# Kernel optimization log

Measured on AMD Instinct MI355X. Metric: run time of the kernel, lower is better.

The kernel has to match this reference:

```python
import jax, jax.numpy as jnp
import numpy as np

B, T, D, L = 16, 2048, 512, 2


def setup_inputs() -> dict:
    key = jax.random.key(0)
    k1, k2, k3 = jax.random.split(key, 3)
    scale = 1.0 / np.sqrt(D)
    x = jax.random.normal(k1, (B, T, D), dtype=jnp.float32)
    Wx = jax.random.normal(k2, (L, D, 4 * D), dtype=jnp.float32) * scale
    Wh = jax.random.normal(k3, (L, D, 4 * D), dtype=jnp.float32) * scale
    b = jnp.zeros((L, 4 * D), dtype=jnp.float32)
    return {"x": x, "Wx": Wx, "Wh": Wh, "b": b}


def _lstm_layer(y, Wx_l, Wh_l, b_l):
    # y: [B, T, D]; Wx_l: [D, 4D]; Wh_l: [D, 4D]; b_l: [4D]
    Bn, Tn, Dn = y.shape
    # Precompute input contribution for all timesteps (one big GEMM).
    xg = jnp.einsum('btd,de->bte', y, Wx_l) + b_l  # [B, T, 4D]

    def step(carry, xt):
        h, c = carry
        gates = xt + h @ Wh_l  # [B, 4D]
        i, f, g, o = jnp.split(gates, 4, axis=-1)
        i = jax.nn.sigmoid(i)
        f = jax.nn.sigmoid(f)
        g = jnp.tanh(g)
        o = jax.nn.sigmoid(o)
        c = f * c + i * g
        h = o * jnp.tanh(c)
        return (h, c), h

    h0 = jnp.zeros((Bn, Dn), y.dtype)
    c0 = jnp.zeros((Bn, Dn), y.dtype)
    _, ys = jax.lax.scan(step, (h0, c0), jnp.swapaxes(xg, 0, 1))  # [T, B, D]
    return jnp.swapaxes(ys, 0, 1)


def reference(x, Wx, Wh, b):
    # Stacked LSTM with residual skip (flax LSTMCell gate order i, f, g, o;
    # input kernels have no bias, hidden kernels carry the bias -> single b).
    y = x
    for l in range(Wx.shape[0]):
        y = _lstm_layer(y, Wx[l], Wh[l], b[l])
    return y + x  # skip=1
```

## Files before the change

### kernel.cpp

```cpp
#include <hip/hip_runtime.h>
#include <stdint.h>

#define B_  16
#define T_  2048
#define D_  512

typedef short v8s __attribute__((ext_vector_type(8)));
typedef float v4f __attribute__((ext_vector_type(4)));

#define WT_OFF   0u
#define H0_OFF   8388608u
#define H1_OFF   41943040u
#define XB_OFF   75497472u
#define WS_NEED  (XB_OFF + 33554432u)

#define SENT 0xFFFFFFFFu

__device__ __forceinline__ short f2bf(float f) {
  unsigned u = __builtin_bit_cast(unsigned, f);
  u = (u + 0x7FFFu + ((u >> 16) & 1u)) >> 16;
  return (short)u;
}
__device__ __forceinline__ float sigmoid_fast(float z) { return 1.f / (1.f + __expf(-z)); }
__device__ __forceinline__ float tanh_fast(float z) {
  float e = __expf(2.f * z);
  return 1.f - 2.f / (e + 1.f);
}
__device__ __forceinline__ unsigned long long cohLoadU2(const unsigned* p) {
  return __hip_atomic_load((unsigned long long*)p, __ATOMIC_RELAXED, __HIP_MEMORY_SCOPE_AGENT);
}
__device__ __forceinline__ void cohStoreU(unsigned* p, unsigned v) {
  __hip_atomic_store(p, v, __ATOMIC_RELAXED, __HIP_MEMORY_SCOPE_AGENT);
}

__global__ void prep_weights(const float* __restrict__ Wx, const float* __restrict__ Wh,
                             short* __restrict__ wT) {
  int tid = blockIdx.x * 256 + threadIdx.x;
  int l   = tid >> 21;
  int mat = (tid >> 20) & 1;
  int rem = tid & ((1 << 20) - 1);
  int k   = rem >> 11;
  int col = rem & 2047;
  const float* src = mat ? Wh : Wx;
  float v = src[(l << 20) + (k << 11) + col];
  int q = col >> 9, r9 = col & 511, g = r9 >> 3, jj = r9 & 7;
  int c = q * 8 + jj, ntile = c >> 4, n = c & 15;
  int kap = k >> 5, k5 = k & 31, quad = k5 >> 3, j = k5 & 7;
  int lane = quad * 16 + n;
  int dst = ((((l * 2 + mat) * 64 + g) * 2 + ntile) * 16 + kap) * 512 + lane * 8 + j;
  wT[dst] = f2bf(v);
}

__global__ void prep_x(const float* __restrict__ x, short* __restrict__ xP,
                       unsigned* __restrict__ hwords) {
  int tid = blockIdx.x * 256 + threadIdx.x;
  hwords[tid] = SENT;
  int b = tid >> 20, r = tid & ((1 << 20) - 1), t = r >> 9, d = r & 511;
  xP[(size_t)t * 8192 + (d >> 3) * 128 + b * 8 + (d & 7)] = f2bf(x[tid]);
}

__device__ __forceinline__ unsigned coh_load8(const short* p, v8s afr[8]) {
  unsigned mx = 0;
#pragma unroll
  for (int kk = 0; kk < 8; ++kk) {
    const unsigned* q = (const unsigned*)(p + kk * 512);
    unsigned long long w0 = cohLoadU2(q);
    unsigned long long w1 = cohLoadU2(q + 2);
    unsigned a = (unsigned)w0, b = (unsigned)(w0 >> 32);
    unsigned c = (unsigned)w1, d = (unsigned)(w1 >> 32);
    mx = a > mx ? a : mx;
    mx = b > mx ? b : mx;
    mx = c > mx ? c : mx;
    mx = d > mx ? d : mx;
    uint4 pk; pk.x = a; pk.y = b; pk.z = c; pk.w = d;
    afr[kk] = __builtin_bit_cast(v8s, pk);
  }
  return mx;
}

__device__ __forceinline__ void mfma32(const v8s afr[8], const v8s wfr[4][8], v4f acc[4]) {
#pragma unroll
  for (int kk = 0; kk < 8; ++kk) {
#pragma unroll
    for (int nt = 0; nt < 4; ++nt)
      acc[nt] = __builtin_amdgcn_mfma_f32_16x16x32_bf16(afr[kk], wfr[nt][kk], acc[nt], 0, 0, 0);
  }
}

__global__ __launch_bounds__(256, 1) void lstm_persist(
    const float* __restrict__ x, const short* __restrict__ xP,
    const short* __restrict__ wT, const float* __restrict__ bias,
    short* h0, short* h1, float* __restrict__ out) {
  const int wg   = blockIdx.x;
  const int l    = wg >> 5;
  const int g    = wg & 31;
  const int tid  = threadIdx.x;
  const int wave = tid >> 6;
  const int lane = tid & 63;
  const int m    = wave >> 1;
  const int kh   = wave & 1;
  const int n15  = lane & 15;
  const int quad = lane >> 4;

  __shared__ float LDSG[2][4][16][68];

  short* hOwn = l ? h1 : h0;

  v8s wfr[4][8];
#pragma unroll
  for (int nt = 0; nt < 4; ++nt) {
    const int gOld = 2 * g + (nt >> 1);
    const int nt2  = nt & 1;
    const short* wb = wT + (size_t)((((l * 2 + m) * 64 + gOld) * 2 + nt2) * 16 + kh * 8) * 512 + lane * 8;
#pragma unroll
    for (int kk = 0; kk < 8; ++kk) wfr[nt][kk] = *(const v8s*)(wb + kk * 512);
  }

  const int eIdx = wave * 64 + lane;
  const int bb = eIdx >> 3, jp = eIdx & 7;
  const int hi = jp >> 2;
  const int jj = 2 * (jp & 3);
  float bq[4][2];
#pragma unroll
  for (int q = 0; q < 4; ++q) {
    bq[q][0] = bias[l * 2048 + q * 512 + g * 16 + 2 * jp];
    bq[q][1] = bias[l * 2048 + q * 512 + g * 16 + 2 * jp + 1];
  }
  float c0 = 0.f, c1 = 0.f;

  const int aOff = kh * 4096 + quad * 128 + n15 * 8;

  for (int t = 0; t < T_; ++t) {
    const int buf = t & 1;

    float2 xv;
    size_t xi = 0;
    if (l == 1 && wave < 2) {
      xi = (size_t)bb * (T_ * D_) + (size_t)t * D_ + g * 16 + 2 * jp;
      xv = *(const float2*)(x + xi);
    }

    v4f acc[4];
#pragma unroll
    for (int nt = 0; nt < 4; ++nt) acc[nt] = (v4f){0.f, 0.f, 0.f, 0.f};

    const short* hp = nullptr;
    if (m == 0) {
      if (l == 0) {
        const short* p = xP + (size_t)t * 8192 + aOff;
        v8s afr[8];
#pragma unroll
        for (int kk = 0; kk < 8; ++kk) afr[kk] = *(const v8s*)(p + kk * 512);
        mfma32(afr, wfr, acc);
      } else {
        hp = h0 + (size_t)t * 8192 + aOff;
      }
    } else if (t > 0) {
      hp = hOwn + (size_t)(t - 1) * 8192 + aOff;
    }

    if (hp) {
      v8s afr[8];
      unsigned mx = coh_load8(hp, afr);
      mfma32(afr, wfr, acc);
      if (__ballot(mx == SENT) != 0) {
        do {
          __builtin_amdgcn_s_sleep(1);
          mx = coh_load8(hp, afr);
        } while (__ballot(mx == SENT) != 0);
#pragma unroll
        for (int nt = 0; nt < 4; ++nt) acc[nt] = (v4f){0.f, 0.f, 0.f, 0.f};
        mfma32(afr, wfr, acc);
      }
    }

#pragma unroll
    for (int nt = 0; nt < 4; ++nt) {
      const int rb = quad * 4;
#pragma unroll
      for (int r = 0; r < 4; ++r)
        LDSG[buf][wave][rb + r][nt * 16 + n15] = acc[nt][r];
    }
    __syncthreads();

    if (wave < 2) {
      float2 s[4];
#pragma unroll
      for (int q = 0; q < 4; ++q) {
        const int coff = (hi * 2 + (q >> 1)) * 16 + (q & 1) * 8 + jj;
        float2 a0 = *(const float2*)&LDSG[buf][0][bb][coff];
        float2 a1 = *(const float2*)&LDSG[buf][1][bb][coff];
        float2 a2 = *(const float2*)&LDSG[buf][2][bb][coff];
        float2 a3 = *(const float2*)&LDSG[buf][3][bb][coff];
        s[q].x = a0.x + a1.x + a2.x + a3.x + bq[q][0];
        s[q].y = a0.y + a1.y + a2.y + a3.y + bq[q][1];
      }
      float i0 = sigmoid_fast(s[0].x), i1 = sigmoid_fast(s[0].y);
      float f0 = sigmoid_fast(s[1].x), f1 = sigmoid_fast(s[1].y);
      float g0 = tanh_fast(s[2].x),    g1 = tanh_fast(s[2].y);
      float o0 = sigmoid_fast(s[3].x), o1 = sigmoid_fast(s[3].y);
      c0 = f0 * c0 + i0 * g0;
      c1 = f1 * c1 + i1 * g1;
      float h0v = o0 * tanh_fast(c0);
      float h1v = o1 * tanh_fast(c1);
      unsigned pack = (unsigned)(unsigned short)f2bf(h0v) |
                      ((unsigned)(unsigned short)f2bf(h1v) << 16);
      cohStoreU((unsigned*)hOwn + (size_t)t * 4096 + (2 * g + hi) * 64 + bb * 4 + (jp & 3), pack);
      if (l == 1) {
        float2 ov; ov.x = h0v + xv.x; ov.y = h1v + xv.y;
        *(float2*)(out + xi) = ov;
      }
    }
  }
}

extern "C" void kernel_launch(void* const* d_in, const int* in_sizes, int n_in,
                              void* d_out, int out_size, void* d_ws, size_t ws_size,
                              hipStream_t stream) {
  const float* x    = (const float*)d_in[0];
  const float* Wx   = (const float*)d_in[1];
  const float* Wh   = (const float*)d_in[2];
  const float* bias = (const float*)d_in[3];
  float* out = (float*)d_out;

  char* ws   = (char*)d_ws;
  short* wT  = (short*)(ws + WT_OFF);
  short* h0  = (short*)(ws + H0_OFF);
  short* h1  = (short*)(ws + H1_OFF);
  short* xP  = (short*)(ws + XB_OFF);
  unsigned* hwords = (unsigned*)(ws + H0_OFF);

  hipLaunchKernelGGL(prep_weights, dim3(16384), dim3(256), 0, stream, Wx, Wh, wT);
  hipLaunchKernelGGL(prep_x, dim3(65536), dim3(256), 0, stream, x, xP, hwords);
  hipLaunchKernelGGL(lstm_persist, dim3(64), dim3(256), 0, stream,
                     x, xP, wT, bias, h0, h1, out);
}
```

Baseline: 5.093 ms.

## Add XCC-local ring buffer handoff with runtime handshake and prefetch of layer-0 h

```diff
diff --git a/kernel.cpp b/kernel.cpp
--- a/kernel.cpp
+++ b/kernel.cpp
@@ -7,12 +7,13 @@
 
 typedef short v8s __attribute__((ext_vector_type(8)));
 typedef float v4f __attribute__((ext_vector_type(4)));
-
-#define WT_OFF   0u
-#define H0_OFF   8388608u
-#define H1_OFF   41943040u
-#define XB_OFF   75497472u
-#define WS_NEED  (XB_OFF + 33554432u)
+typedef unsigned u32x4 __attribute__((ext_vector_type(4)));
+
+#define WT_OFF    0u
+#define H0_OFF    8388608u
+#define H1_OFF    41943040u
+#define XB_OFF    75497472u
+#define SLACK_OFF 109051904u
 
 #define SENT 0xFFFFFFFFu
 
@@ -26,11 +27,20 @@
   float e = __expf(2.f * z);
   return 1.f - 2.f / (e + 1.f);
 }
+__device__ __forceinline__ unsigned cohLoadU(const unsigned* p) {
+  return __hip_atomic_load((unsigned*)p, __ATOMIC_RELAXED, __HIP_MEMORY_SCOPE_AGENT);
+}
 __device__ __forceinline__ unsigned long long cohLoadU2(const unsigned* p) {
   return __hip_atomic_load((unsigned long long*)p, __ATOMIC_RELAXED, __HIP_MEMORY_SCOPE_AGENT);
 }
 __device__ __forceinline__ void cohStoreU(unsigned* p, unsigned v) {
   __hip_atomic_store(p, v, __ATOMIC_RELAXED, __HIP_MEMORY_SCOPE_AGENT);
+}
+__device__ __forceinline__ unsigned sc0LoadU(const unsigned* p) {
+  unsigned v;
+  asm volatile("global_load_dword %0, %1, off sc0\n\ts_waitcnt vmcnt(0)"
+               : "=v"(v) : "v"(p) : "memory");
+  return v;
 }
 
 __global__ void prep_weights(const float* __restrict__ Wx, const float* __restrict__ Wh,
@@ -52,9 +62,10 @@
 }
 
 __global__ void prep_x(const float* __restrict__ x, short* __restrict__ xP,
-                       unsigned* __restrict__ hwords) {
+                       unsigned* __restrict__ hwords, unsigned* __restrict__ slack) {
   int tid = blockIdx.x * 256 + threadIdx.x;
   hwords[tid] = SENT;
+  if (tid < 1024) slack[tid] = SENT;
   int b = tid >> 20, r = tid & ((1 << 20) - 1), t = r >> 9, d = r & 511;
   xP[(size_t)t * 8192 + (d >> 3) * 128 + b * 8 + (d & 7)] = f2bf(x[tid]);
 }
@@ -78,7 +89,7 @@
   return mx;
 }
 
-__device__ __forceinline__ void mfma32(const v8s afr[8], const v8s wfr[4][8], v4f acc[4]) {
+__device__ __forceinline__ void mfma32(const v8s afr[8], const v8s (&wfr)[4][8], v4f (&acc)[4]) {
 #pragma unroll
   for (int kk = 0; kk < 8; ++kk) {
 #pragma unroll
@@ -87,13 +98,29 @@
   }
 }
 
+__device__ __forceinline__ void agent_consume(const short* hp, const v8s (&wfr)[4][8], v4f (&acc)[4]) {
+  v8s a[8];
+  unsigned mx = coh_load8(hp, a);
+  mfma32(a, wfr, acc);
+  if (__ballot(mx == SENT) != 0) {
+    do {
+      __builtin_amdgcn_s_sleep(1);
+      mx = coh_load8(hp, a);
+    } while (__ballot(mx == SENT) != 0);
+#pragma unroll
+    for (int nt = 0; nt < 4; ++nt) acc[nt] = (v4f){0.f, 0.f, 0.f, 0.f};
+    mfma32(a, wfr, acc);
+  }
+}
+
 __global__ __launch_bounds__(256, 1) void lstm_persist(
     const float* __restrict__ x, const short* __restrict__ xP,
-    const short* __restrict__ wT, const float* __restrict__ bias,
-    short* h0, short* h1, float* __restrict__ out) {
-  const int wg   = blockIdx.x;
-  const int l    = wg >> 5;
-  const int g    = wg & 31;
+    const short* wT, const float* __restrict__ bias,
+    short* h0, short* h1, float* __restrict__ out, char* ws) {
+  const int wg = blockIdx.x;
+  if ((wg & 7) >= 2) return;
+  const int l = wg & 7;
+  const int g = wg >> 3;
   const int tid  = threadIdx.x;
   const int wave = tid >> 6;
   const int lane = tid & 63;
@@ -102,9 +129,14 @@
   const int n15  = lane & 15;
   const int quad = lane >> 4;
 
-  __shared__ float LDSG[2][4][16][68];
+  __shared__ float LDSG[2][4][16][76];
+  __shared__ int HS;
 
   short* hOwn = l ? h1 : h0;
+  unsigned* hLinW = (unsigned*)hOwn;
+  unsigned* ringOwn = (unsigned*)(ws + WT_OFF) + (size_t)l * (1u << 20);
+  unsigned* hsT = (unsigned*)(ws + SLACK_OFF);
+  const int wid = l * 32 + g;
 
   v8s wfr[4][8];
 #pragma unroll
@@ -115,7 +147,6 @@
 #pragma unroll
     for (int kk = 0; kk < 8; ++kk) wfr[nt][kk] = *(const v8s*)(wb + kk * 512);
   }
-
   const int eIdx = wave * 64 + lane;
   const int bb = eIdx >> 3, jp = eIdx & 7;
   const int hi = jp >> 2;
@@ -126,9 +157,52 @@
     bq[q][0] = bias[l * 2048 + q * 512 + g * 16 + 2 * jp];
     bq[q][1] = bias[l * 2048 + q * 512 + g * 16 + 2 * jp + 1];
   }
+  asm volatile("s_waitcnt vmcnt(0)" ::: "memory");
+
+  if (wave == 0) {
+    unsigned myxcc;
+    asm volatile("s_getreg_b32 %0, hwreg(20, 0, 32)" : "=s"(myxcc));
+    myxcc &= 0xFFu;
+    if (lane == 0) {
+#pragma unroll
+      for (int r = 0; r < 4; ++r) hsT[r * 64 + wid] = 0xA5A50000u + r;
+      cohStoreU(&hsT[256 + wid], 0xB0000000u | myxcc);
+    }
+    bool mine = true;
+    if (lane < 32) {
+      const int p = l * 32 + lane;
+      unsigned long long dl = __builtin_amdgcn_s_memrealtime() + 400000ull;
+      for (;;) {
+        bool ok = true;
+#pragma unroll
+        for (int r = 0; r < 4; ++r) ok = ok && (sc0LoadU(&hsT[r * 64 + p]) == 0xA5A50000u + r);
+        ok = ok && (cohLoadU(&hsT[256 + p]) == (0xB0000000u | myxcc));
+        if (ok) break;
+        if (__builtin_amdgcn_s_memrealtime() > dl) { mine = false; break; }
+        __builtin_amdgcn_s_sleep(2);
+      }
+    }
+    const bool myBit = (__ballot(mine ? 1 : 0) == ~0ull);
+    if (lane == 0) cohStoreU(&hsT[320 + wid], 0xC0000000u | (myBit ? 1u : 0u));
+    bool agree = true;
+    if (lane < 32) {
+      const int p = l * 32 + lane;
+      unsigned v;
+      do { v = cohLoadU(&hsT[320 + p]); if (v == SENT) __builtin_amdgcn_s_sleep(2); } while (v == SENT);
+      agree = (v & 1u) != 0u;
+    }
+    const bool fastLayer = (__ballot(agree ? 1 : 0) == ~0ull);
+    if (lane == 0) HS = fastLayer ? 1 : 0;
+  }
+  __syncthreads();
+  const bool fastL = (HS != 0);
+
   float c0 = 0.f, c1 = 0.f;
-
-  const int aOff = kh * 4096 + quad * 128 + n15 * 8;
+  const int aOff  = kh * 4096 + quad * 128 + n15 * 8;
+  const int wOffA = kh * 2048 + quad * 64 + n15 * 4;
+  bool useFast = fastL;
+  int fails = 0;
+  u32x4 pf[8];
 
   for (int t = 0; t < T_; ++t) {
     const int buf = t & 1;
@@ -144,7 +218,6 @@
 #pragma unroll
     for (int nt = 0; nt < 4; ++nt) acc[nt] = (v4f){0.f, 0.f, 0.f, 0.f};
 
-    const short* hp = nullptr;
     if (m == 0) {
       if (l == 0) {
         const short* p = xP + (size_t)t * 8192 + aOff;
@@ -153,25 +226,73 @@
         for (int kk = 0; kk < 8; ++kk) afr[kk] = *(const v8s*)(p + kk * 512);
         mfma32(afr, wfr, acc);
       } else {
-        hp = h0 + (size_t)t * 8192 + aOff;
+        bool ok = false;
+        if (t > 0) {
+          unsigned mx = 0;
+#pragma unroll
+          for (int kk = 0; kk < 8; ++kk) {
+            unsigned a_ = pf[kk].x > pf[kk].y ? pf[kk].x : pf[kk].y;
+            unsigned b_ = pf[kk].z > pf[kk].w ? pf[kk].z : pf[kk].w;
+            unsigned m_ = a_ > b_ ? a_ : b_;
+            mx = m_ > mx ? m_ : mx;
+          }
+          if (__ballot(mx == SENT) == 0ull) {
+            v8s a[8];
+#pragma unroll
+            for (int kk = 0; kk < 8; ++kk) a[kk] = __builtin_bit_cast(v8s, pf[kk]);
+            mfma32(a, wfr, acc);
+            ok = true;
+          }
+        }
+        if (!ok) agent_consume(h0 + (size_t)t * 8192 + aOff, wfr, acc);
+        if (t + 1 < T_) {
+          const unsigned* q = (const unsigned*)(h0 + (size_t)(t + 1) * 8192 + aOff);
+#pragma unroll
+          for (int kk = 0; kk < 8; ++kk) {
+            unsigned long long w0 = cohLoadU2(q + kk * 256);
+            unsigned long long w1 = cohLoadU2(q + kk * 256 + 2);
+            u32x4 v; v.x = (unsigned)w0; v.y = (unsigned)(w0 >> 32);
+            v.z = (unsigned)w1; v.w = (unsigned)(w1 >> 32);
+            pf[kk] = v;
+          }
+        }
       }
     } else if (t > 0) {
-      hp = hOwn + (size_t)(t - 1) * 8192 + aOff;
-    }
-
-    if (hp) {
-      v8s afr[8];
-      unsigned mx = coh_load8(hp, afr);
-      mfma32(afr, wfr, acc);
-      if (__ballot(mx == SENT) != 0) {
-        do {
-          __builtin_amdgcn_s_sleep(1);
-          mx = coh_load8(hp, afr);
-        } while (__ballot(mx == SENT) != 0);
-#pragma unroll
-        for (int nt = 0; nt < 4; ++nt) acc[nt] = (v4f){0.f, 0.f, 0.f, 0.f};
-        mfma32(afr, wfr, acc);
-      }
+      bool got = false;
+      if (useFast && t >= 129) {
+        const unsigned* rp = ringOwn + (unsigned)((t - 1) & 255) * 4096 + wOffA;
+        for (int pass = 0; pass < 64; ++pass) {
+          u32x4 u[8];
+#pragma unroll
+          for (int kk = 0; kk < 8; ++kk) {
+            const unsigned* p = rp + kk * 256;
+            asm volatile("global_load_dwordx4 %0, %1, off sc0" : "=v"(u[kk]) : "v"(p) : "memory");
+          }
+          asm volatile("s_waitcnt vmcnt(0)" ::: "memory");
+          __builtin_amdgcn_sched_barrier(0);
+          unsigned mx = 0;
+#pragma unroll
+          for (int kk = 0; kk < 8; ++kk) {
+            unsigned a_ = u[kk].x > u[kk].y ? u[kk].x : u[kk].y;
+            unsigned b_ = u[kk].z > u[kk].w ? u[kk].z : u[kk].w;
+            unsigned m_ = a_ > b_ ? a_ : b_;
+            mx = m_ > mx ? m_ : mx;
+          }
+          if (__ballot(mx == SENT) == 0ull) {
+#pragma unroll
+            for (int kk = 0; kk < 8; ++kk) {
+              v8s a_ = __builtin_bit_cast(v8s, u[kk]);
+#pragma unroll
+              for (int nt = 0; nt < 4; ++nt)
+                acc[nt] = __builtin_amdgcn_mfma_f32_16x16x32_bf16(a_, wfr[nt][kk], acc[nt], 0, 0, 0);
+            }
+            got = true;
+            break;
+          }
+        }
+        if (!got) { if (++fails > 16) useFast = false; }
+      }
+      if (!got) agent_consume(hOwn + (size_t)(t - 1) * 8192 + aOff, wfr, acc);
     }
 
 #pragma unroll
@@ -205,7 +326,12 @@
       float h1v = o1 * tanh_fast(c1);
       unsigned pack = (unsigned)(unsigned short)f2bf(h0v) |
                       ((unsigned)(unsigned short)f2bf(h1v) << 16);
-      cohStoreU((unsigned*)hOwn + (size_t)t * 4096 + (2 * g + hi) * 64 + bb * 4 + (jp & 3), pack);
+      const unsigned woff = (2u * g + hi) * 64 + bb * 4 + (jp & 3);
+      cohStoreU(hLinW + (size_t)t * 4096 + woff, pack);
+      if (fastL && t >= 8) {
+        ringOwn[(unsigned)(t & 255) * 4096 + woff] = pack;
+        ringOwn[(unsigned)((t + 120) & 255) * 4096 + woff] = SENT;
+      }
       if (l == 1) {
         float2 ov; ov.x = h0v + xv.x; ov.y = h1v + xv.y;
         *(float2*)(out + xi) = ov;
@@ -229,9 +355,10 @@
   short* h1  = (short*)(ws + H1_OFF);
   short* xP  = (short*)(ws + XB_OFF);
   unsigned* hwords = (unsigned*)(ws + H0_OFF);
+  unsigned* slack  = (unsigned*)(ws + SLACK_OFF);
 
   hipLaunchKernelGGL(prep_weights, dim3(16384), dim3(256), 0, stream, Wx, Wh, wT);
-  hipLaunchKernelGGL(prep_x, dim3(65536), dim3(256), 0, stream, x, xP, hwords);
-  hipLaunchKernelGGL(lstm_persist, dim3(64), dim3(256), 0, stream,
-                     x, xP, wT, bias, h0, h1, out);
-}
+  hipLaunchKernelGGL(prep_x, dim3(65536), dim3(256), 0, stream, x, xP, hwords, slack);
+  hipLaunchKernelGGL(lstm_persist, dim3(256), dim3(256), 0, stream,
+                     x, xP, wT, bias, h0, h1, out, ws);
+}
```

After: 9.279 ms. +82.2%, slower.
